# Kernel tuning notes

Hardware: AMD Instinct MI355X
Metric: run time of the kernel (lower is better)

Reference implementation:

```python
import jax, jax.numpy as jnp
import numpy as np

N = 50000      # num_nodes
R = 8          # num_relations
FIN = 128      # in_channels
H = 128        # hidden_channels
E = 800000     # num_edges (avg degree 16)


def _xavier(key, shape):
    fan_in, fan_out = shape[-2], shape[-1]
    lim = np.sqrt(6.0 / (fan_in + fan_out)).astype(np.float32)
    return jax.random.uniform(key, shape, jnp.float32, -lim, lim)


def setup_inputs() -> dict:
    key = jax.random.key(0)
    ks = jax.random.split(key, 10)
    return {
        "x": jax.random.normal(ks[0], (N, FIN), jnp.float32),
        "edge_index": jax.random.randint(ks[1], (2, E), 0, N, jnp.int32),
        "edge_type": jax.random.randint(ks[2], (E,), 0, R, jnp.int32),
        "rel_w0": _xavier(ks[3], (R, FIN, H)),
        "root_w0": _xavier(ks[4], (FIN, H)),
        "bias0": jnp.zeros((H,), jnp.float32),
        "rel_w1": _xavier(ks[5], (R, H, H)),
        "root_w1": _xavier(ks[6], (H, H)),
        "bias1": jnp.zeros((H,), jnp.float32),
        "rel_emb": _xavier(ks[7], (R, H)),
    }


def _rgcn_conv(x, src, dst, etype, rel_w, root_w, bias):
    # RGCNConv (PyG, aggr='mean'): out_i = root(x_i) + sum_r W_r * mean_{j in N_r(i)} x_j
    n = x.shape[0]
    seg = dst * R + etype                                   # fused (node, relation) segment id
    msgs = x[src]                                           # [E, F] gather
    sums = jax.ops.segment_sum(msgs, seg, num_segments=n * R)
    cnt = jax.ops.segment_sum(jnp.ones((src.shape[0], 1), x.dtype), seg, num_segments=n * R)
    mean = (sums / jnp.maximum(cnt, 1.0)).reshape(n, R, -1)  # [N, R, F]
    return jnp.einsum('nrf,rfh->nh', mean, rel_w) + x @ root_w + bias


def reference(x, edge_index, edge_type, rel_w0, root_w0, bias0,
              rel_w1, root_w1, bias1, rel_emb):
    src, dst = edge_index[0], edge_index[1]
    h = _rgcn_conv(x, src, dst, edge_type, rel_w0, root_w0, bias0)
    h = jax.nn.relu(h)  # dropout in eval mode (identity)
    h = _rgcn_conv(h, src, dst, edge_type, rel_w1, root_w1, bias1)
    return (h, rel_emb)
```

## Files before the change

kernel.cpp:

```cpp
#include <hip/hip_runtime.h>

typedef unsigned short ushort_t;
typedef __attribute__((ext_vector_type(8))) short short8;
typedef __attribute__((ext_vector_type(4))) float f32x4;
typedef __attribute__((ext_vector_type(4))) int int4v;

#define RNUM 8
#define FDIM 128

__device__ __forceinline__ float bf2f(ushort_t u) {
    union { unsigned int i; float f; } x;
    x.i = ((unsigned int)u) << 16;
    return x.f;
}
__device__ __forceinline__ ushort_t f2bf(float f) {
    union { float f; unsigned int i; } x;
    x.f = f;
    unsigned int u = x.i;
    u += 0x7fffu + ((u >> 16) & 1u);
    return (ushort_t)(u >> 16);
}


__global__ void init_head(int* __restrict__ head, int n) {
    int i = blockIdx.x * 256 + threadIdx.x;
    if (i < n) head[i] = -1;
}

__global__ void link_kernel(const int* __restrict__ src, const int* __restrict__ dst,
                            const int* __restrict__ et,
                            int* head, int2* __restrict__ meta, int E) {
    int i = blockIdx.x * 256 + threadIdx.x;
    if (i < E) {
        int seg = dst[i] * RNUM + et[i];
        int prev = atomicExch(&head[seg * 4 + (i & 3)], i);
        meta[i] = make_int2(src[i], prev);
    }
}


__global__ __launch_bounds__(256) void transpose_w(const float* __restrict__ rel_w,
                                                   const float* __restrict__ root_w,
                                                   ushort_t* __restrict__ Wt) {
    int r = blockIdx.x;
    const float* src = (r < 8) ? (rel_w + r * 16384) : root_w;
    __shared__ ushort_t t[128 * 130];
    for (int idx = threadIdx.x; idx < 16384; idx += 256)
        t[(idx >> 7) * 130 + (idx & 127)] = f2bf(src[idx]);
    __syncthreads();
    ushort_t* d = Wt + r * 16384;
    for (int idx = threadIdx.x; idx < 16384; idx += 256)
        d[idx] = t[(idx & 127) * 130 + (idx >> 7)];
}


__global__ void cast_x(const float* __restrict__ x, ushort_t* __restrict__ xc,
                       int total, int totalPad) {
    int i = (blockIdx.x * 256 + threadIdx.x) * 8;
    if (i >= totalPad) return;
    ushort_t o[8];
    if (i < total) {
        float4 v0 = *(const float4*)(x + i);
        float4 v1 = *(const float4*)(x + i + 4);
        o[0] = f2bf(v0.x); o[1] = f2bf(v0.y); o[2] = f2bf(v0.z); o[3] = f2bf(v0.w);
        o[4] = f2bf(v1.x); o[5] = f2bf(v1.y); o[6] = f2bf(v1.z); o[7] = f2bf(v1.w);
    } else {
#pragma unroll
        for (int k = 0; k < 8; ++k) o[k] = 0;
    }
    *(int4v*)(xc + i) = *(int4v*)o;
}


__global__ __launch_bounds__(256) void seg_mean(const int4v* __restrict__ head4,
                                                const int2* __restrict__ meta,
                                                const ushort_t* __restrict__ X,
                                                ushort_t* __restrict__ Mm,
                                                int NSEG) {
    int t = blockIdx.x * 256 + threadIdx.x;
    int seg = t >> 4;
    int l16 = t & 15;
    if (seg >= NSEG) return;
    const ushort_t* gbase = X + l16 * 8;

    float acc[8];
#pragma unroll
    for (int k = 0; k < 8; ++k) acc[k] = 0.f;

    int4v h4 = head4[seg];
    int j[4], s[4], n[4];
#pragma unroll
    for (int c = 0; c < 4; ++c) j[c] = h4[c];
#pragma unroll
    for (int c = 0; c < 4; ++c)
        if (j[c] >= 0) { int2 m = meta[j[c]]; s[c] = m.x; n[c] = m.y; }

    int cnt = 0;
    while ((j[0] & j[1] & j[2] & j[3]) >= 0) {
        int4v v[4];
#pragma unroll
        for (int c = 0; c < 4; ++c)
            if (j[c] >= 0) v[c] = *(const int4v*)(gbase + ((size_t)s[c] << 7));
        int2 m2[4];
#pragma unroll
        for (int c = 0; c < 4; ++c)
            if (j[c] >= 0 && n[c] >= 0) m2[c] = meta[n[c]];
#pragma unroll
        for (int c = 0; c < 4; ++c) {
            if (j[c] >= 0) {
                const ushort_t* p = (const ushort_t*)&v[c];
#pragma unroll
                for (int k = 0; k < 8; ++k) acc[k] += bf2f(p[k]);
                ++cnt;
                j[c] = n[c];
                s[c] = m2[c].x;
                n[c] = m2[c].y;
            }
        }
    }

    float sc = (cnt > 0) ? 1.0f / (float)cnt : 0.f;
    ushort_t ov[8];
#pragma unroll
    for (int k = 0; k < 8; ++k) ov[k] = f2bf(acc[k] * sc);
    *(int4v*)(Mm + ((size_t)seg << 7) + l16 * 8) = *(int4v*)ov;
}


template <bool FINAL>
__global__ __launch_bounds__(256, 2) void rgcn_gemm(
    const ushort_t* __restrict__ Mm,
    const ushort_t* __restrict__ Xc,
    const ushort_t* __restrict__ Wt,
    const float* __restrict__ bias, float* __restrict__ outF,
    ushort_t* __restrict__ Xout, int N) {
    __shared__ ushort_t As[128 * 128];
    __shared__ ushort_t Bs[128 * 128];
    int tid = threadIdx.x;
    int wid = tid >> 6, lane = tid & 63;
    int l16 = lane & 15, q = lane >> 4;
    int nodeBase = blockIdx.x * 128;

    f32x4 acc[2][8];
#pragma unroll
    for (int rt = 0; rt < 2; ++rt)
#pragma unroll
        for (int ct = 0; ct < 8; ++ct) acc[rt][ct] = (f32x4){0.f, 0.f, 0.f, 0.f};

    int4v aReg[8], bReg[8];

    auto issueLoads = [&](int r) {
#pragma unroll
        for (int i = 0; i < 8; ++i) {
            int L = i * 256 + tid;
            int row = L >> 4;
            int c = (L & 15) ^ (row & 15);
            const ushort_t* ga = (r < 8)
                ? Mm + ((size_t)(nodeBase + row) << 10) + r * 128 + c * 8
                : Xc + ((size_t)(nodeBase + row) << 7) + c * 8;
            aReg[i] = *(const int4v*)ga;
            bReg[i] = *(const int4v*)(Wt + r * 16384 + row * 128 + c * 8);
        }
    };
    auto writeLds = [&]() {
#pragma unroll
        for (int i = 0; i < 8; ++i) {
            int L = i * 256 + tid;
            *(int4v*)((char*)As + (size_t)L * 16) = aReg[i];
            *(int4v*)((char*)Bs + (size_t)L * 16) = bReg[i];
        }
    };

    issueLoads(0);
    writeLds();
    __syncthreads();

    for (int r = 0; r < 9; ++r) {
        if (r < 8) issueLoads(r + 1);
#pragma unroll
        for (int s = 0; s < 4; ++s) {
            int pos = ((s * 4 + q) ^ l16) * 16;
            short8 a0 = *(const short8*)((const char*)As + ((2 * wid + 0) * 16 + l16) * 256 + pos);
            short8 a1 = *(const short8*)((const char*)As + ((2 * wid + 1) * 16 + l16) * 256 + pos);
#pragma unroll
            for (int ct = 0; ct < 8; ++ct) {
                short8 b = *(const short8*)((const char*)Bs + (ct * 16 + l16) * 256 + pos);
                acc[0][ct] = __builtin_amdgcn_mfma_f32_16x16x32_bf16(a0, b, acc[0][ct], 0, 0, 0);
                acc[1][ct] = __builtin_amdgcn_mfma_f32_16x16x32_bf16(a1, b, acc[1][ct], 0, 0, 0);
            }
        }
        __syncthreads();
        if (r < 8) {
            writeLds();
            __syncthreads();
        }
    }

#pragma unroll
    for (int rt = 0; rt < 2; ++rt) {
#pragma unroll
        for (int ct = 0; ct < 8; ++ct) {
            int h = ct * 16 + l16;
            float bv = bias[h];
#pragma unroll
            for (int reg = 0; reg < 4; ++reg) {
                int node = nodeBase + (2 * wid + rt) * 16 + q * 4 + reg;
                float v = acc[rt][ct][reg] + bv;
                if (FINAL) {
                    if (node < N) outF[(size_t)node * FDIM + h] = v;
                } else {
                    Xout[(size_t)node * FDIM + h] =
                        (node < N) ? f2bf(fmaxf(v, 0.f)) : (ushort_t)0;
                }
            }
        }
    }
}

__global__ void copy_emb(const float* __restrict__ e, float* __restrict__ out, int n) {
    int i = blockIdx.x * 256 + threadIdx.x;
    if (i < n) out[i] = e[i];
}


extern "C" void kernel_launch(void* const* d_in, const int* in_sizes, int n_in,
                              void* d_out, int out_size, void* d_ws, size_t ws_size,
                              hipStream_t stream) {
    const float* x        = (const float*)d_in[0];
    const int* edge_index = (const int*)d_in[1];
    const int* edge_type  = (const int*)d_in[2];
    const float* rel_w0   = (const float*)d_in[3];
    const float* root_w0  = (const float*)d_in[4];
    const float* bias0    = (const float*)d_in[5];
    const float* rel_w1   = (const float*)d_in[6];
    const float* root_w1  = (const float*)d_in[7];
    const float* bias1    = (const float*)d_in[8];
    const float* rel_emb  = (const float*)d_in[9];

    int N = in_sizes[0] / FDIM;
    int E = in_sizes[1] / 2;
    int NSEG = N * RNUM;
    const int* src = edge_index;
    const int* dst = edge_index + E;

    int nb_gemm = (N + 127) / 128;
    int NPAD = nb_gemm * 128;

    char* w = (char*)d_ws;
    auto alloc = [&](size_t bytes) -> char* {
        char* p = w;
        w += (bytes + 255) & ~(size_t)255;
        return p;
    };
    int* head     = (int*)alloc((size_t)NSEG * 4 * 4);
    int2* meta    = (int2*)alloc((size_t)E * 8);
    ushort_t* Wt  = (ushort_t*)alloc((size_t)2 * 9 * 16384 * 2);
    ushort_t* xc  = (ushort_t*)alloc((size_t)NPAD * FDIM * 2);
    ushort_t* h1c = (ushort_t*)alloc((size_t)NPAD * FDIM * 2);
    ushort_t* Mm  = (ushort_t*)alloc((size_t)NPAD * RNUM * FDIM * 2);
    (void)ws_size; (void)n_in; (void)out_size;

    int nb_head = (NSEG * 4 + 255) / 256;
    int nb_E    = (E + 255) / 256;
    int nb_mean = (NSEG * 16) / 256;
    int nb_cast = (NPAD * FDIM) / (256 * 8);

    init_head<<<nb_head, 256, 0, stream>>>(head, NSEG * 4);
    link_kernel<<<nb_E, 256, 0, stream>>>(src, dst, edge_type, head, meta, E);
    transpose_w<<<9, 256, 0, stream>>>(rel_w0, root_w0, Wt);
    transpose_w<<<9, 256, 0, stream>>>(rel_w1, root_w1, Wt + 9 * 16384);
    cast_x<<<nb_cast, 256, 0, stream>>>(x, xc, N * FDIM, NPAD * FDIM);

    seg_mean<<<nb_mean, 256, 0, stream>>>((const int4v*)head, meta, xc, Mm, NSEG);
    rgcn_gemm<false><<<nb_gemm, 256, 0, stream>>>(Mm, xc, Wt, bias0, nullptr, h1c, N);
    seg_mean<<<nb_mean, 256, 0, stream>>>((const int4v*)head, meta, h1c, Mm, NSEG);
    rgcn_gemm<true><<<nb_gemm, 256, 0, stream>>>(Mm, h1c, Wt + 9 * 16384, bias1,
                                                 (float*)d_out, nullptr, N);
    copy_emb<<<4, 256, 0, stream>>>(rel_emb, (float*)d_out + (size_t)N * FDIM,
                                    in_sizes[9]);
}
```

Before: 321.0 us.

## Use 8 waves per GEMM block and merge the two weight-transpose launches

The relational GEMM block grows from 256 to 512 threads, so each of its 8 waves computes one 16-row tile instead of two, which halves per-thread accumulator and staging registers. The launch bound is raised to target 4 blocks per CU for more latency hiding. Separately, the two weight-transpose launches are merged into one 18-block launch to save a kernel launch. Each wave now reuses its A fragment over fewer MFMAs, which raises the LDS read traffic for B per MFMA. The 64KB of LDS per block may also cap occupancy below the launch-bound target.

```diff
diff --git a/kernel.cpp b/kernel.cpp
--- a/kernel.cpp
+++ b/kernel.cpp
@@ -39,16 +39,22 @@
 }
 
 
-__global__ __launch_bounds__(256) void transpose_w(const float* __restrict__ rel_w,
-                                                   const float* __restrict__ root_w,
+__global__ __launch_bounds__(256) void transpose_w(const float* __restrict__ rel_w0,
+                                                   const float* __restrict__ root_w0,
+                                                   const float* __restrict__ rel_w1,
+                                                   const float* __restrict__ root_w1,
                                                    ushort_t* __restrict__ Wt) {
-    int r = blockIdx.x;
-    const float* src = (r < 8) ? (rel_w + r * 16384) : root_w;
+    int b = blockIdx.x;
+    int layer = (b >= 9) ? 1 : 0;
+    int r = b - layer * 9;
+    const float* rel  = layer ? rel_w1 : rel_w0;
+    const float* root = layer ? root_w1 : root_w0;
+    const float* src = (r < 8) ? (rel + r * 16384) : root;
     __shared__ ushort_t t[128 * 130];
     for (int idx = threadIdx.x; idx < 16384; idx += 256)
         t[(idx >> 7) * 130 + (idx & 127)] = f2bf(src[idx]);
     __syncthreads();
-    ushort_t* d = Wt + r * 16384;
+    ushort_t* d = Wt + (layer * 9 + r) * 16384;
     for (int idx = threadIdx.x; idx < 16384; idx += 256)
         d[idx] = t[(idx & 127) * 130 + (idx >> 7)];
 }
@@ -128,7 +134,7 @@
 
 
 template <bool FINAL>
-__global__ __launch_bounds__(256, 2) void rgcn_gemm(
+__global__ __launch_bounds__(512, 4) void rgcn_gemm(
     const ushort_t* __restrict__ Mm,
     const ushort_t* __restrict__ Xc,
     const ushort_t* __restrict__ Wt,
@@ -137,22 +143,20 @@
     __shared__ ushort_t As[128 * 128];
     __shared__ ushort_t Bs[128 * 128];
     int tid = threadIdx.x;
-    int wid = tid >> 6, lane = tid & 63;
+    int wv = tid >> 6, lane = tid & 63;
     int l16 = lane & 15, q = lane >> 4;
     int nodeBase = blockIdx.x * 128;
 
-    f32x4 acc[2][8];
-#pragma unroll
-    for (int rt = 0; rt < 2; ++rt)
-#pragma unroll
-        for (int ct = 0; ct < 8; ++ct) acc[rt][ct] = (f32x4){0.f, 0.f, 0.f, 0.f};
-
-    int4v aReg[8], bReg[8];
+    f32x4 acc[8];
+#pragma unroll
+    for (int ct = 0; ct < 8; ++ct) acc[ct] = (f32x4){0.f, 0.f, 0.f, 0.f};
+
+    int4v aReg[4], bReg[4];
 
     auto issueLoads = [&](int r) {
 #pragma unroll
-        for (int i = 0; i < 8; ++i) {
-            int L = i * 256 + tid;
+        for (int i = 0; i < 4; ++i) {
+            int L = i * 512 + tid;
             int row = L >> 4;
             int c = (L & 15) ^ (row & 15);
             const ushort_t* ga = (r < 8)
@@ -164,8 +168,8 @@
     };
     auto writeLds = [&]() {
 #pragma unroll
-        for (int i = 0; i < 8; ++i) {
-            int L = i * 256 + tid;
+        for (int i = 0; i < 4; ++i) {
+            int L = i * 512 + tid;
             *(int4v*)((char*)As + (size_t)L * 16) = aReg[i];
             *(int4v*)((char*)Bs + (size_t)L * 16) = bReg[i];
         }
@@ -180,13 +184,11 @@
 #pragma unroll
         for (int s = 0; s < 4; ++s) {
             int pos = ((s * 4 + q) ^ l16) * 16;
-            short8 a0 = *(const short8*)((const char*)As + ((2 * wid + 0) * 16 + l16) * 256 + pos);
-            short8 a1 = *(const short8*)((const char*)As + ((2 * wid + 1) * 16 + l16) * 256 + pos);
+            short8 a = *(const short8*)((const char*)As + (wv * 16 + l16) * 256 + pos);
 #pragma unroll
             for (int ct = 0; ct < 8; ++ct) {
                 short8 b = *(const short8*)((const char*)Bs + (ct * 16 + l16) * 256 + pos);
-                acc[0][ct] = __builtin_amdgcn_mfma_f32_16x16x32_bf16(a0, b, acc[0][ct], 0, 0, 0);
-                acc[1][ct] = __builtin_amdgcn_mfma_f32_16x16x32_bf16(a1, b, acc[1][ct], 0, 0, 0);
+                acc[ct] = __builtin_amdgcn_mfma_f32_16x16x32_bf16(a, b, acc[ct], 0, 0, 0);
             }
         }
         __syncthreads();
@@ -197,21 +199,18 @@
     }
 
 #pragma unroll
-    for (int rt = 0; rt < 2; ++rt) {
-#pragma unroll
-        for (int ct = 0; ct < 8; ++ct) {
-            int h = ct * 16 + l16;
-            float bv = bias[h];
-#pragma unroll
-            for (int reg = 0; reg < 4; ++reg) {
-                int node = nodeBase + (2 * wid + rt) * 16 + q * 4 + reg;
-                float v = acc[rt][ct][reg] + bv;
-                if (FINAL) {
-                    if (node < N) outF[(size_t)node * FDIM + h] = v;
-                } else {
-                    Xout[(size_t)node * FDIM + h] =
-                        (node < N) ? f2bf(fmaxf(v, 0.f)) : (ushort_t)0;
-                }
+    for (int ct = 0; ct < 8; ++ct) {
+        int h = ct * 16 + l16;
+        float bv = bias[h];
+#pragma unroll
+        for (int reg = 0; reg < 4; ++reg) {
+            int node = nodeBase + wv * 16 + q * 4 + reg;
+            float v = acc[ct][reg] + bv;
+            if (FINAL) {
+                if (node < N) outF[(size_t)node * FDIM + h] = v;
+            } else {
+                Xout[(size_t)node * FDIM + h] =
+                    (node < N) ? f2bf(fmaxf(v, 0.f)) : (ushort_t)0;
             }
         }
     }
@@ -267,14 +266,13 @@
 
     init_head<<<nb_head, 256, 0, stream>>>(head, NSEG * 4);
     link_kernel<<<nb_E, 256, 0, stream>>>(src, dst, edge_type, head, meta, E);
-    transpose_w<<<9, 256, 0, stream>>>(rel_w0, root_w0, Wt);
-    transpose_w<<<9, 256, 0, stream>>>(rel_w1, root_w1, Wt + 9 * 16384);
+    transpose_w<<<18, 256, 0, stream>>>(rel_w0, root_w0, rel_w1, root_w1, Wt);
     cast_x<<<nb_cast, 256, 0, stream>>>(x, xc, N * FDIM, NPAD * FDIM);
 
     seg_mean<<<nb_mean, 256, 0, stream>>>((const int4v*)head, meta, xc, Mm, NSEG);
-    rgcn_gemm<false><<<nb_gemm, 256, 0, stream>>>(Mm, xc, Wt, bias0, nullptr, h1c, N);
+    rgcn_gemm<false><<<nb_gemm, 512, 0, stream>>>(Mm, xc, Wt, bias0, nullptr, h1c, N);
     seg_mean<<<nb_mean, 256, 0, stream>>>((const int4v*)head, meta, h1c, Mm, NSEG);
-    rgcn_gemm<true><<<nb_gemm, 256, 0, stream>>>(Mm, h1c, Wt + 9 * 16384, bias1,
+    rgcn_gemm<true><<<nb_gemm, 512, 0, stream>>>(Mm, h1c, Wt + 9 * 16384, bias1,
                                                  (float*)d_out, nullptr, N);
     copy_emb<<<4, 256, 0, stream>>>(rel_emb, (float*)d_out + (size_t)N * FDIM,
                                     in_sizes[9]);
```

Result: no change. 315.2 us (-1.8%).
